# Kernel optimization log

Measured on AMD Instinct MI355X. Metric: run time of the kernel, lower is better.

## Reference

```python
import jax, jax.numpy as jnp
import numpy as np
import math

B, S, HID, H = 2, 4096, 512, 8
D_K = HID // H


def setup_inputs() -> dict:
    key = jax.random.key(0)
    ks = jax.random.split(key, 8)
    inp = {
        "query": jax.random.normal(ks[0], (B, S, HID), dtype=jnp.float32),
        "key": jax.random.normal(ks[1], (B, S, HID), dtype=jnp.float32),
        "value": jax.random.normal(ks[2], (B, S, HID), dtype=jnp.float32),
        "mask": jax.random.randint(ks[3], (B, S), 0, 2, dtype=jnp.int32),
        # conv1d kernel_size=1, bias=False -> plain [out,in] weights (xavier-normal-ish)
        "Wq": jax.random.normal(ks[4], (HID, HID), dtype=jnp.float32) * (1.0 / math.sqrt(HID)),
        "Wk": jax.random.normal(ks[5], (HID, HID), dtype=jnp.float32) * (1.0 / math.sqrt(HID)),
        "Wv": jax.random.normal(ks[6], (HID, HID), dtype=jnp.float32) * (1.0 / math.sqrt(HID)),
        "Wo": jax.random.normal(ks[7], (HID, HID), dtype=jnp.float32) * (1.0 / math.sqrt(HID)),
    }
    return inp


def reference(query, key, value, mask, Wq, Wk, Wv, Wo):
    b, s, _ = query.shape
    # conv1d(k=1, bias=False) projection == x @ W.T; split heads -> [b,h,s,d_k]
    def proj(x, W):
        return jnp.einsum('bsd,ed->bse', x, W).reshape(b, s, H, D_K).transpose(0, 2, 1, 3)
    q, k, v = proj(query, Wq), proj(key, Wk), proj(value, Wv)
    # NOTE: original scales by 1/log(d_k), not 1/sqrt(d_k)
    score = jnp.einsum('bhqd,bhkd->bhqk', q, k) / math.log(D_K)
    m = mask.reshape(b, 1, 1, s)  # broadcast over heads and query positions
    score = jnp.where(m == 0, jnp.float32(-1e30), score)
    attn = jax.nn.softmax(score, axis=-1)  # dropout is identity in eval
    x = jnp.einsum('bhqk,bhkd->bhqd', attn, v)
    x = x.transpose(0, 2, 1, 3).reshape(b, s, HID)
    return jnp.einsum('bsd,ed->bse', x, Wo)
```

## Files before the change

kernel.cpp:

```cpp
#include <hip/hip_runtime.h>
#include <hip/hip_bf16.h>
#include <cstdint>
#include <cstddef>


namespace {

constexpr int kB = 2, kS = 4096, kHid = 512, kH = 8, kDk = 64;
constexpr int kBH = kB * kH;
constexpr int kM = kB * kS;

typedef __attribute__((ext_vector_type(8))) short short8;
typedef __attribute__((ext_vector_type(4))) float floatx4;
typedef __attribute__((ext_vector_type(16))) float floatx16;
typedef __attribute__((ext_vector_type(4))) unsigned int uintx4;
typedef unsigned short u16;

__device__ __forceinline__ u16 bf16rne(float f) {
    uint32_t u = __float_as_uint(f);
    u += 0x7fffu + ((u >> 16) & 1u);
    return (u16)(u >> 16);
}
__device__ __forceinline__ uint32_t pk2(float lo, float hi) {
#if __has_builtin(__builtin_amdgcn_cvt_pk_bf16_f32)
    typedef __attribute__((ext_vector_type(2))) __bf16 bf2;
    bf2 h = __builtin_amdgcn_cvt_pk_bf16_f32(lo, hi);
    return __builtin_bit_cast(uint32_t, h);
#else
    return ((uint32_t)bf16rne(hi) << 16) | (uint32_t)bf16rne(lo);
#endif
}
__device__ __forceinline__ float fexp2(float x) {
#if __has_builtin(__builtin_amdgcn_exp2f)
    return __builtin_amdgcn_exp2f(x);
#else
    return exp2f(x);
#endif
}
__device__ __forceinline__ float bf2f(u16 v) {
    return __uint_as_float((uint32_t)v << 16);
}
__device__ __forceinline__ void plswap(uint32_t& a, uint32_t& b) {
#if __has_builtin(__builtin_amdgcn_permlane32_swap)
    typedef __attribute__((ext_vector_type(2))) unsigned int uint2v;
    uint2v r = __builtin_amdgcn_permlane32_swap(a, b, false, false);
    a = r[0]; b = r[1];
#else
    asm volatile("v_permlane32_swap_b32 %0, %1" : "+v"(a), "+v"(b));
#endif
}
__device__ __forceinline__ void gload16(const void* g, void* l) {
    __builtin_amdgcn_global_load_lds(
        (const __attribute__((address_space(1))) void*)g,
        (__attribute__((address_space(3))) void*)l, 16, 0, 0);
}

__global__ __launch_bounds__(256) void cvt_qw(const float* __restrict__ q,
    const float* __restrict__ k, const float* __restrict__ v,
    const float* __restrict__ w0, const float* __restrict__ w1,
    const float* __restrict__ w2, const float* __restrict__ w3,
    u16* __restrict__ xall, u16* __restrict__ wall) {
    const int bx = blockIdx.x;
    if (bx < 12288) {
        int z = bx >> 12;
        size_t i = (size_t)(bx & 4095) * 256 + threadIdx.x;
        const float* src = z == 0 ? q : (z == 1 ? k : v);
        float4 f = ((const float4*)src)[i];
        ushort4 o;
        o.x = bf16rne(f.x); o.y = bf16rne(f.y);
        o.z = bf16rne(f.z); o.w = bf16rne(f.w);
        ((ushort4*)(xall + (size_t)z * kM * kHid))[i] = o;
    } else {
        int r = bx - 12288;
        int z = r >> 8;
        size_t i = (size_t)(r & 255) * 256 + threadIdx.x;
        const float* src = z == 0 ? w0 : (z == 1 ? w1 : (z == 2 ? w2 : w3));
        float sc = (z == 0)
            ? (float)(1.4426950408889634 / (6.0 * 0.6931471805599453))
            : 1.0f;
        float4 f = ((const float4*)src)[i];
        ushort4 o;
        o.x = bf16rne(f.x * sc); o.y = bf16rne(f.y * sc);
        o.z = bf16rne(f.z * sc); o.w = bf16rne(f.w * sc);
        ((ushort4*)(wall + (size_t)z * kHid * kHid))[i] = o;
    }
}

__global__ __launch_bounds__(256) void cvt_mask(const int* __restrict__ mask,
    float* __restrict__ fb) {
    int i = blockIdx.x * 256 + threadIdx.x;
    fb[i] = mask[i] ? 0.0f : -1e30f;
}

__global__ __launch_bounds__(256, 3) void proj(const u16* __restrict__ xall,
    const u16* __restrict__ wall, u16* __restrict__ qp, u16* __restrict__ kp,
    u16* __restrict__ vt) {
    __shared__ float smt[4][16][68];
    const int z = blockIdx.z;
    const u16* x = xall + (size_t)z * kM * kHid;
    const u16* w = wall + (size_t)z * kHid * kHid;
    const int wv = threadIdx.x >> 6, lane = threadIdx.x & 63;
    const int quad = lane >> 4, l16 = lane & 15;
    const int mb = blockIdx.y * 128 + (wv >> 1) * 64;
    const int nb = blockIdx.x * 128 + (wv & 1) * 64;
    floatx4 acc[4][4] = {};
    const u16* xr = x + (size_t)(mb + l16) * kHid + quad * 8;
    const u16* wr = w + (size_t)(nb + l16) * kHid + quad * 8;
    for (int k0 = 0; k0 < kHid; k0 += 32) {
        short8 a[4], bt[4];
#pragma unroll
        for (int i = 0; i < 4; i++)
            a[i] = *(const short8*)(xr + (size_t)i * 16 * kHid + k0);
#pragma unroll
        for (int t = 0; t < 4; t++)
            bt[t] = *(const short8*)(wr + (size_t)t * 16 * kHid + k0);
#pragma unroll
        for (int i = 0; i < 4; i++)
#pragma unroll
        for (int t = 0; t < 4; t++)
            acc[i][t] = __builtin_amdgcn_mfma_f32_16x16x32_bf16(a[i], bt[t], acc[i][t], 0, 0, 0);
    }
    if (z < 2) {
        u16* dst = (z == 0) ? qp : kp;
        const int row16 = lane >> 2, cseg = (lane & 3) * 16;
#pragma unroll
        for (int i = 0; i < 4; i++) {
#pragma unroll
            for (int t = 0; t < 4; t++)
#pragma unroll
            for (int r = 0; r < 4; r++)
                smt[wv][quad * 4 + r][t * 16 + l16] = acc[i][t][r];
            __builtin_amdgcn_wave_barrier();
            const float* rp = &smt[wv][row16][cseg];
            float4 f0 = *(const float4*)(rp);
            float4 f1 = *(const float4*)(rp + 4);
            float4 f2 = *(const float4*)(rp + 8);
            float4 f3 = *(const float4*)(rp + 12);
            uint4 o0, o1;
            o0.x = pk2(f0.x, f0.y); o0.y = pk2(f0.z, f0.w);
            o0.z = pk2(f1.x, f1.y); o0.w = pk2(f1.z, f1.w);
            o1.x = pk2(f2.x, f2.y); o1.y = pk2(f2.z, f2.w);
            o1.z = pk2(f3.x, f3.y); o1.w = pk2(f3.z, f3.w);
            u16* dp = dst + (size_t)(mb + i * 16 + row16) * kHid + nb + cseg;
            *(uint4*)dp = o0;
            *(uint4*)(dp + 8) = o1;
            __builtin_amdgcn_wave_barrier();
        }
    } else {
#pragma unroll
        for (int i = 0; i < 4; i++)
#pragma unroll
        for (int t = 0; t < 4; t++) {
            int m0 = mb + i * 16 + quad * 4;
            int n = nb + t * 16 + l16;
            int b = m0 >> 12, s = m0 & (kS - 1);
            int h = n >> 6,   d = n & (kDk - 1);
            ushort4 o;
            o.x = bf16rne(acc[i][t][0]); o.y = bf16rne(acc[i][t][1]);
            o.z = bf16rne(acc[i][t][2]); o.w = bf16rne(acc[i][t][3]);
            *(ushort4*)(vt + ((size_t)(b * kH + h) * kDk + d) * kS + s) = o;
        }
    }
}

__global__ __launch_bounds__(256, 4) void attn(const u16* __restrict__ qp,
    const u16* __restrict__ kp, const u16* __restrict__ vt,
    const float* __restrict__ fbias, u16* __restrict__ ows,
    float* __restrict__ rsws) {
    union SmT {
        struct { u16 K[2][64][64]; u16 V[2][64][64]; } s;
        float ep[4][32][33];
    };
    __shared__ __align__(16) SmT sm;
    const int tid = threadIdx.x;
    const int wv = tid >> 6, l = tid & 63;
    const int hf = l >> 5, q32 = l & 31, l7 = l & 7;
    const int bh = blockIdx.y, b = bh >> 3, h = bh & 7;
    const int kz = blockIdx.z;
    const int q0 = blockIdx.x * 128 + wv * 32;
    const u16* Qb = qp + (size_t)b * kS * kHid + h * 64;
    const u16* Kb = kp + (size_t)b * kS * kHid + h * 64;
    const u16* Vb = vt + (size_t)bh * kDk * kS;
    const float* fm = fbias + b * kS;

    short8 qf[4];
#pragma unroll
    for (int m = 0; m < 4; m++)
        qf[m] = *(const short8*)(Qb + (size_t)(q0 + q32) * kHid + m * 16 + hf * 8);

    floatx16 O0 = {}, O1 = {};
    float rs = 0.0f;

    const int srow = l >> 3;
    const int swcol = (l7 ^ srow) * 8;
    auto stage = [&](int itn, int ph) {
        const size_t kr = (size_t)(itn * 64 + wv * 8 + srow);
        gload16(Kb + kr * kHid + swcol,        &sm.s.K[ph][wv * 8][0]);
        gload16(Kb + (kr + 32) * kHid + swcol, &sm.s.K[ph][wv * 8 + 32][0]);
        const size_t vr = (size_t)(wv * 8 + srow) * kS + itn * 64 + swcol;
        gload16(Vb + vr,                       &sm.s.V[ph][wv * 8][0]);
        gload16(Vb + (size_t)32 * kS + vr,     &sm.s.V[ph][wv * 8 + 32][0]);
    };

    stage(kz, 0);
    __syncthreads();

    for (int s = 0; s < 32; ++s) {
        const int it = kz + 2 * s, ph = s & 1, kt = it * 64;
        if (s < 31) stage(it + 2, ph ^ 1);
#pragma unroll
        for (int ks = 0; ks < 2; ++ks) {
            short8 kf[4];
#pragma unroll
            for (int m = 0; m < 4; m++)
                kf[m] = *(const short8*)&sm.s.K[ph][ks * 32 + q32][((2 * m + hf) ^ l7) * 8];
            short8 vf[2][2];
#pragma unroll
            for (int ds = 0; ds < 2; ds++)
#pragma unroll
            for (int tt = 0; tt < 2; tt++)
                vf[ds][tt] = *(const short8*)&sm.s.V[ph][ds * 32 + q32][((ks * 4 + tt * 2 + hf) ^ l7) * 8];
            floatx16 st;
            {
                const float* fp = fm + kt + ks * 32 + 4 * hf;
                float4 g0 = *(const float4*)(fp);
                float4 g1 = *(const float4*)(fp + 8);
                float4 g2 = *(const float4*)(fp + 16);
                float4 g3 = *(const float4*)(fp + 24);
                st[0] = g0.x;  st[1] = g0.y;  st[2] = g0.z;  st[3] = g0.w;
                st[4] = g1.x;  st[5] = g1.y;  st[6] = g1.z;  st[7] = g1.w;
                st[8] = g2.x;  st[9] = g2.y;  st[10] = g2.z; st[11] = g2.w;
                st[12] = g3.x; st[13] = g3.y; st[14] = g3.z; st[15] = g3.w;
            }
#pragma unroll
            for (int m = 0; m < 4; m++)
                st = __builtin_amdgcn_mfma_f32_32x32x16_bf16(kf[m], qf[m], st, 0, 0, 0);
            float xx[16];
#pragma unroll
            for (int r = 0; r < 16; r++) xx[r] = fexp2(st[r]);
            rs += (((xx[0] + xx[1]) + (xx[2] + xx[3])) + ((xx[4] + xx[5]) + (xx[6] + xx[7])))
                + (((xx[8] + xx[9]) + (xx[10] + xx[11])) + ((xx[12] + xx[13]) + (xx[14] + xx[15])));
            uint32_t w00 = pk2(xx[0], xx[1]),   w01 = pk2(xx[2], xx[3]);
            uint32_t w10 = pk2(xx[4], xx[5]),   w11 = pk2(xx[6], xx[7]);
            uint32_t w20 = pk2(xx[8], xx[9]),   w21 = pk2(xx[10], xx[11]);
            uint32_t w30 = pk2(xx[12], xx[13]), w31 = pk2(xx[14], xx[15]);
            plswap(w00, w10); plswap(w01, w11);
            plswap(w20, w30); plswap(w21, w31);
            uintx4 t0 = {w00, w01, w10, w11};
            uintx4 t1 = {w20, w21, w30, w31};
            short8 bf0 = __builtin_bit_cast(short8, t0);
            short8 bf1 = __builtin_bit_cast(short8, t1);
            O0 = __builtin_amdgcn_mfma_f32_32x32x16_bf16(vf[0][0], bf0, O0, 0, 0, 0);
            O0 = __builtin_amdgcn_mfma_f32_32x32x16_bf16(vf[0][1], bf1, O0, 0, 0, 0);
            O1 = __builtin_amdgcn_mfma_f32_32x32x16_bf16(vf[1][0], bf0, O1, 0, 0, 0);
            O1 = __builtin_amdgcn_mfma_f32_32x32x16_bf16(vf[1][1], bf1, O1, 0, 0, 0);
        }
        __syncthreads();
    }

    rs += __shfl_xor(rs, 32);
    if (hf == 0)
        rsws[((size_t)kz * kBH + bh) * kS + q0 + q32] = rs;

    u16* Ob = ows + (((size_t)kz * kBH + bh) * kS + q0) * kDk;
#pragma unroll
    for (int ds = 0; ds < 2; ds++) {
#pragma unroll
        for (int r = 0; r < 16; r++)
            sm.ep[wv][q32][(r & 3) + 8 * (r >> 2) + 4 * hf] = (ds == 0) ? O0[r] : O1[r];
        __builtin_amdgcn_wave_barrier();
        {
            const int qq = l >> 1, c0 = (l & 1) * 16;
            float f[16];
#pragma unroll
            for (int j = 0; j < 16; j++) f[j] = sm.ep[wv][qq][c0 + j];
            uint4 o0, o1;
            o0.x = pk2(f[0], f[1]);   o0.y = pk2(f[2], f[3]);
            o0.z = pk2(f[4], f[5]);   o0.w = pk2(f[6], f[7]);
            o1.x = pk2(f[8], f[9]);   o1.y = pk2(f[10], f[11]);
            o1.z = pk2(f[12], f[13]); o1.w = pk2(f[14], f[15]);
            u16* dp = Ob + (size_t)qq * kDk + ds * 32 + c0;
            *(uint4*)dp = o0;
            *(uint4*)(dp + 8) = o1;
        }
        __builtin_amdgcn_wave_barrier();
    }
}

__global__ __launch_bounds__(256) void combine(const u16* __restrict__ ows,
    const float* __restrict__ rsws, u16* __restrict__ xo) {
    size_t i = (size_t)blockIdx.x * 256 + threadIdx.x;
    const int d8 = (int)(i & 7);
    const int s  = (int)((i >> 3) & (kS - 1));
    const int bh = (int)(i >> 15);
    const int b = bh >> 3, h = bh & 7;
    const size_t base = ((size_t)bh * kS + s) * kDk + d8 * 8;
    short8 a = *(const short8*)(ows + base);
    short8 c = *(const short8*)(ows + (size_t)kBH * kS * kDk + base);
    float r = rsws[(size_t)bh * kS + s] + rsws[(size_t)kBH * kS + (size_t)bh * kS + s];
    float inv = 1.0f / r;
    float e[8];
#pragma unroll
    for (int j = 0; j < 8; j++)
        e[j] = (bf2f((u16)a[j]) + bf2f((u16)c[j])) * inv;
    uint4 o;
    o.x = pk2(e[0], e[1]); o.y = pk2(e[2], e[3]);
    o.z = pk2(e[4], e[5]); o.w = pk2(e[6], e[7]);
    *(uint4*)(xo + ((size_t)b * kS + s) * kHid + h * 64 + d8 * 8) = o;
}

__global__ __launch_bounds__(256, 3) void oproj(const u16* __restrict__ x,
    const u16* __restrict__ w, float* __restrict__ out) {
    const int wv = threadIdx.x >> 6, lane = threadIdx.x & 63;
    const int quad = lane >> 4, l16 = lane & 15;
    const int mb = blockIdx.y * 128 + (wv >> 1) * 64;
    const int nb = blockIdx.x * 128 + (wv & 1) * 64;
    floatx4 acc[4][4] = {};
    const u16* xr = x + (size_t)(mb + l16) * kHid + quad * 8;
    const u16* wr = w + (size_t)(nb + l16) * kHid + quad * 8;
    for (int k0 = 0; k0 < kHid; k0 += 32) {
        short8 a[4], bt[4];
#pragma unroll
        for (int i = 0; i < 4; i++)
            a[i] = *(const short8*)(xr + (size_t)i * 16 * kHid + k0);
#pragma unroll
        for (int t = 0; t < 4; t++)
            bt[t] = *(const short8*)(wr + (size_t)t * 16 * kHid + k0);
#pragma unroll
        for (int i = 0; i < 4; i++)
#pragma unroll
        for (int t = 0; t < 4; t++)
            acc[i][t] = __builtin_amdgcn_mfma_f32_16x16x32_bf16(a[i], bt[t], acc[i][t], 0, 0, 0);
    }
#pragma unroll
    for (int i = 0; i < 4; i++)
#pragma unroll
    for (int t = 0; t < 4; t++)
#pragma unroll
    for (int r = 0; r < 4; r++) {
        int m = mb + i * 16 + quad * 4 + r;
        int n = nb + t * 16 + l16;
        out[(size_t)m * kHid + n] = acc[i][t][r];
    }
}

}

extern "C" void kernel_launch(void* const* d_in, const int* in_sizes, int n_in,
                              void* d_out, int out_size, void* d_ws, size_t ws_size,
                              hipStream_t stream) {
    const float* q  = (const float*)d_in[0];
    const float* k  = (const float*)d_in[1];
    const float* v  = (const float*)d_in[2];
    const int* mask = (const int*)d_in[3];
    const float* w0 = (const float*)d_in[4];
    const float* w1 = (const float*)d_in[5];
    const float* w2 = (const float*)d_in[6];
    const float* w3 = (const float*)d_in[7];
    float* out = (float*)d_out;

    u16* ws   = (u16*)d_ws;
    u16* xall = ws;
    u16* wall = xall + (size_t)3 * kM * kHid;
    u16* qp   = wall + (size_t)4 * kHid * kHid;
    u16* kp   = qp + (size_t)kBH * kS * kDk;
    u16* vt   = kp + (size_t)kBH * kS * kDk;
    u16* ows  = xall;
    float* fbias = (float*)(xall + (size_t)2 * kM * kHid);
    float* rsws  = fbias + (size_t)kB * kS;
    u16* xo   = qp;

    dim3 blk(256);
    cvt_qw <<<dim3(13312), blk, 0, stream>>>(q, k, v, w0, w1, w2, w3, xall, wall);
    proj   <<<dim3(kHid / 128, kM / 128, 3), blk, 0, stream>>>(xall, wall, qp, kp, vt);
    cvt_mask<<<dim3(kB * kS / 256), blk, 0, stream>>>(mask, fbias);
    attn   <<<dim3(kS / 128, kBH, 2), blk, 0, stream>>>(qp, kp, vt, fbias, ows, rsws);
    combine<<<dim3(2048), blk, 0, stream>>>(ows, rsws, xo);
    oproj  <<<dim3(kHid / 128, kM / 128), blk, 0, stream>>>(
        xo, wall + (size_t)3 * kHid * kHid, out);
}
```

Measured before the change: 268.4 us.

## Process two query tiles per wave in attention to reuse K/V fragments

Each wave now handles 64 query rows (two 32-row tiles) instead of 32, so every K/V tile staged in shared memory and every fragment read from LDS serves twice as many MFMA ops. The grid is flattened to 512 blocks with a remapped block index that interleaves heads and places the two key-split halves in separate block ranges. Stage pointers are advanced incrementally rather than recomputed. In exchange, register pressure roughly doubles, occupancy drops to 2 blocks per CU, and the grid is halved.

```diff
diff --git a/kernel.cpp b/kernel.cpp
--- a/kernel.cpp
+++ b/kernel.cpp
@@ -163,7 +163,7 @@
     }
 }
 
-__global__ __launch_bounds__(256, 4) void attn(const u16* __restrict__ qp,
+__global__ __launch_bounds__(256, 2) void attn(const u16* __restrict__ qp,
     const u16* __restrict__ kp, const u16* __restrict__ vt,
     const float* __restrict__ fbias, u16* __restrict__ ows,
     float* __restrict__ rsws) {
@@ -175,39 +175,47 @@
     const int tid = threadIdx.x;
     const int wv = tid >> 6, l = tid & 63;
     const int hf = l >> 5, q32 = l & 31, l7 = l & 7;
-    const int bh = blockIdx.y, b = bh >> 3, h = bh & 7;
-    const int kz = blockIdx.z;
-    const int q0 = blockIdx.x * 128 + wv * 32;
+    const int wg = blockIdx.x;
+    const int bh = ((wg & 7) << 1) | ((wg >> 3) & 1);
+    const int qb = (wg >> 4) & 15;
+    const int kz = wg >> 8;
+    const int b = bh >> 3, h = bh & 7;
+    const int qbase = qb * 256 + wv * 64;
     const u16* Qb = qp + (size_t)b * kS * kHid + h * 64;
     const u16* Kb = kp + (size_t)b * kS * kHid + h * 64;
     const u16* Vb = vt + (size_t)bh * kDk * kS;
     const float* fm = fbias + b * kS;
 
-    short8 qf[4];
+    short8 qf[2][4];
+#pragma unroll
+    for (int qt = 0; qt < 2; qt++)
 #pragma unroll
     for (int m = 0; m < 4; m++)
-        qf[m] = *(const short8*)(Qb + (size_t)(q0 + q32) * kHid + m * 16 + hf * 8);
-
-    floatx16 O0 = {}, O1 = {};
-    float rs = 0.0f;
+        qf[qt][m] = *(const short8*)(Qb + (size_t)(qbase + qt * 32 + q32) * kHid + m * 16 + hf * 8);
+
+    floatx16 O[2][2] = {};
+    float rs[2] = {0.0f, 0.0f};
 
     const int srow = l >> 3;
-    const int swcol = (l7 ^ srow) * 8;
-    auto stage = [&](int itn, int ph) {
-        const size_t kr = (size_t)(itn * 64 + wv * 8 + srow);
-        gload16(Kb + kr * kHid + swcol,        &sm.s.K[ph][wv * 8][0]);
-        gload16(Kb + (kr + 32) * kHid + swcol, &sm.s.K[ph][wv * 8 + 32][0]);
-        const size_t vr = (size_t)(wv * 8 + srow) * kS + itn * 64 + swcol;
-        gload16(Vb + vr,                       &sm.s.V[ph][wv * 8][0]);
-        gload16(Vb + (size_t)32 * kS + vr,     &sm.s.V[ph][wv * 8 + 32][0]);
+    const int pcol = (l7 ^ srow) * 8;
+    const u16* pK = Kb + (size_t)(kz * 64 + wv * 8 + srow) * kHid + pcol;
+    const u16* pV = Vb + (size_t)(wv * 8 + srow) * kS + kz * 64 + pcol;
+    auto stage = [&](int ph) {
+        gload16(pK,                        &sm.s.K[ph][wv * 8][0]);
+        gload16(pK + (size_t)32 * kHid,    &sm.s.K[ph][wv * 8 + 32][0]);
+        gload16(pV,                        &sm.s.V[ph][wv * 8][0]);
+        gload16(pV + (size_t)32 * kS,      &sm.s.V[ph][wv * 8 + 32][0]);
+        pK += (size_t)128 * kHid;
+        pV += 128;
     };
 
-    stage(kz, 0);
+    stage(0);
     __syncthreads();
 
-    for (int s = 0; s < 32; ++s) {
-        const int it = kz + 2 * s, ph = s & 1, kt = it * 64;
-        if (s < 31) stage(it + 2, ph ^ 1);
+    for (int s5 = 0; s5 < 32; ++s5) {
+        const int ph = s5 & 1;
+        const int kt = (kz + 2 * s5) * 64;
+        if (s5 < 31) stage(ph ^ 1);
 #pragma unroll
         for (int ks = 0; ks < 2; ++ks) {
             short8 kf[4];
@@ -220,70 +228,74 @@
 #pragma unroll
             for (int tt = 0; tt < 2; tt++)
                 vf[ds][tt] = *(const short8*)&sm.s.V[ph][ds * 32 + q32][((ks * 4 + tt * 2 + hf) ^ l7) * 8];
-            floatx16 st;
-            {
-                const float* fp = fm + kt + ks * 32 + 4 * hf;
-                float4 g0 = *(const float4*)(fp);
-                float4 g1 = *(const float4*)(fp + 8);
-                float4 g2 = *(const float4*)(fp + 16);
-                float4 g3 = *(const float4*)(fp + 24);
+            const float* fp = fm + kt + ks * 32 + 4 * hf;
+            float4 g0 = *(const float4*)(fp);
+            float4 g1 = *(const float4*)(fp + 8);
+            float4 g2 = *(const float4*)(fp + 16);
+            float4 g3 = *(const float4*)(fp + 24);
+#pragma unroll
+            for (int qt = 0; qt < 2; ++qt) {
+                floatx16 st;
                 st[0] = g0.x;  st[1] = g0.y;  st[2] = g0.z;  st[3] = g0.w;
                 st[4] = g1.x;  st[5] = g1.y;  st[6] = g1.z;  st[7] = g1.w;
                 st[8] = g2.x;  st[9] = g2.y;  st[10] = g2.z; st[11] = g2.w;
                 st[12] = g3.x; st[13] = g3.y; st[14] = g3.z; st[15] = g3.w;
+#pragma unroll
+                for (int m = 0; m < 4; m++)
+                    st = __builtin_amdgcn_mfma_f32_32x32x16_bf16(kf[m], qf[qt][m], st, 0, 0, 0);
+                float xx[16];
+#pragma unroll
+                for (int r = 0; r < 16; r++) xx[r] = fexp2(st[r]);
+                rs[qt] += (((xx[0] + xx[1]) + (xx[2] + xx[3])) + ((xx[4] + xx[5]) + (xx[6] + xx[7])))
+                        + (((xx[8] + xx[9]) + (xx[10] + xx[11])) + ((xx[12] + xx[13]) + (xx[14] + xx[15])));
+                uint32_t w00 = pk2(xx[0], xx[1]),   w01 = pk2(xx[2], xx[3]);
+                uint32_t w10 = pk2(xx[4], xx[5]),   w11 = pk2(xx[6], xx[7]);
+                uint32_t w20 = pk2(xx[8], xx[9]),   w21 = pk2(xx[10], xx[11]);
+                uint32_t w30 = pk2(xx[12], xx[13]), w31 = pk2(xx[14], xx[15]);
+                plswap(w00, w10); plswap(w01, w11);
+                plswap(w20, w30); plswap(w21, w31);
+                uintx4 t0 = {w00, w01, w10, w11};
+                uintx4 t1 = {w20, w21, w30, w31};
+                short8 bf0 = __builtin_bit_cast(short8, t0);
+                short8 bf1 = __builtin_bit_cast(short8, t1);
+                O[qt][0] = __builtin_amdgcn_mfma_f32_32x32x16_bf16(vf[0][0], bf0, O[qt][0], 0, 0, 0);
+                O[qt][0] = __builtin_amdgcn_mfma_f32_32x32x16_bf16(vf[0][1], bf1, O[qt][0], 0, 0, 0);
+                O[qt][1] = __builtin_amdgcn_mfma_f32_32x32x16_bf16(vf[1][0], bf0, O[qt][1], 0, 0, 0);
+                O[qt][1] = __builtin_amdgcn_mfma_f32_32x32x16_bf16(vf[1][1], bf1, O[qt][1], 0, 0, 0);
             }
-#pragma unroll
-            for (int m = 0; m < 4; m++)
-                st = __builtin_amdgcn_mfma_f32_32x32x16_bf16(kf[m], qf[m], st, 0, 0, 0);
-            float xx[16];
-#pragma unroll
-            for (int r = 0; r < 16; r++) xx[r] = fexp2(st[r]);
-            rs += (((xx[0] + xx[1]) + (xx[2] + xx[3])) + ((xx[4] + xx[5]) + (xx[6] + xx[7])))
-                + (((xx[8] + xx[9]) + (xx[10] + xx[11])) + ((xx[12] + xx[13]) + (xx[14] + xx[15])));
-            uint32_t w00 = pk2(xx[0], xx[1]),   w01 = pk2(xx[2], xx[3]);
-            uint32_t w10 = pk2(xx[4], xx[5]),   w11 = pk2(xx[6], xx[7]);
-            uint32_t w20 = pk2(xx[8], xx[9]),   w21 = pk2(xx[10], xx[11]);
-            uint32_t w30 = pk2(xx[12], xx[13]), w31 = pk2(xx[14], xx[15]);
-            plswap(w00, w10); plswap(w01, w11);
-            plswap(w20, w30); plswap(w21, w31);
-            uintx4 t0 = {w00, w01, w10, w11};
-            uintx4 t1 = {w20, w21, w30, w31};
-            short8 bf0 = __builtin_bit_cast(short8, t0);
-            short8 bf1 = __builtin_bit_cast(short8, t1);
-            O0 = __builtin_amdgcn_mfma_f32_32x32x16_bf16(vf[0][0], bf0, O0, 0, 0, 0);
-            O0 = __builtin_amdgcn_mfma_f32_32x32x16_bf16(vf[0][1], bf1, O0, 0, 0, 0);
-            O1 = __builtin_amdgcn_mfma_f32_32x32x16_bf16(vf[1][0], bf0, O1, 0, 0, 0);
-            O1 = __builtin_amdgcn_mfma_f32_32x32x16_bf16(vf[1][1], bf1, O1, 0, 0, 0);
         }
         __syncthreads();
     }
 
-    rs += __shfl_xor(rs, 32);
-    if (hf == 0)
-        rsws[((size_t)kz * kBH + bh) * kS + q0 + q32] = rs;
-
-    u16* Ob = ows + (((size_t)kz * kBH + bh) * kS + q0) * kDk;
-#pragma unroll
-    for (int ds = 0; ds < 2; ds++) {
-#pragma unroll
-        for (int r = 0; r < 16; r++)
-            sm.ep[wv][q32][(r & 3) + 8 * (r >> 2) + 4 * hf] = (ds == 0) ? O0[r] : O1[r];
-        __builtin_amdgcn_wave_barrier();
-        {
-            const int qq = l >> 1, c0 = (l & 1) * 16;
-            float f[16];
-#pragma unroll
-            for (int j = 0; j < 16; j++) f[j] = sm.ep[wv][qq][c0 + j];
-            uint4 o0, o1;
-            o0.x = pk2(f[0], f[1]);   o0.y = pk2(f[2], f[3]);
-            o0.z = pk2(f[4], f[5]);   o0.w = pk2(f[6], f[7]);
-            o1.x = pk2(f[8], f[9]);   o1.y = pk2(f[10], f[11]);
-            o1.z = pk2(f[12], f[13]); o1.w = pk2(f[14], f[15]);
-            u16* dp = Ob + (size_t)qq * kDk + ds * 32 + c0;
-            *(uint4*)dp = o0;
-            *(uint4*)(dp + 8) = o1;
+#pragma unroll
+    for (int qt = 0; qt < 2; ++qt) {
+        float r = rs[qt];
+        r += __shfl_xor(r, 32);
+        if (hf == 0)
+            rsws[((size_t)kz * kBH + bh) * kS + qbase + qt * 32 + q32] = r;
+        u16* Ob = ows + (((size_t)kz * kBH + bh) * kS + qbase + qt * 32) * kDk;
+#pragma unroll
+        for (int ds = 0; ds < 2; ds++) {
+#pragma unroll
+            for (int rr = 0; rr < 16; rr++)
+                sm.ep[wv][q32][(rr & 3) + 8 * (rr >> 2) + 4 * hf] = O[qt][ds][rr];
+            __builtin_amdgcn_wave_barrier();
+            {
+                const int qq = l >> 1, c0 = (l & 1) * 16;
+                float f[16];
+#pragma unroll
+                for (int j = 0; j < 16; j++) f[j] = sm.ep[wv][qq][c0 + j];
+                uint4 o0, o1;
+                o0.x = pk2(f[0], f[1]);   o0.y = pk2(f[2], f[3]);
+                o0.z = pk2(f[4], f[5]);   o0.w = pk2(f[6], f[7]);
+                o1.x = pk2(f[8], f[9]);   o1.y = pk2(f[10], f[11]);
+                o1.z = pk2(f[12], f[13]); o1.w = pk2(f[14], f[15]);
+                u16* dp = Ob + (size_t)qq * kDk + ds * 32 + c0;
+                *(uint4*)dp = o0;
+                *(uint4*)(dp + 8) = o1;
+            }
+            __builtin_amdgcn_wave_barrier();
         }
-        __builtin_amdgcn_wave_barrier();
     }
 }
 
@@ -374,7 +386,7 @@
     cvt_qw <<<dim3(13312), blk, 0, stream>>>(q, k, v, w0, w1, w2, w3, xall, wall);
     proj   <<<dim3(kHid / 128, kM / 128, 3), blk, 0, stream>>>(xall, wall, qp, kp, vt);
     cvt_mask<<<dim3(kB * kS / 256), blk, 0, stream>>>(mask, fbias);
-    attn   <<<dim3(kS / 128, kBH, 2), blk, 0, stream>>>(qp, kp, vt, fbias, ows, rsws);
+    attn   <<<dim3(512), blk, 0, stream>>>(qp, kp, vt, fbias, ows, rsws);
     combine<<<dim3(2048), blk, 0, stream>>>(ows, rsws, xo);
     oproj  <<<dim3(kHid / 128, kM / 128), blk, 0, stream>>>(
         xo, wall + (size_t)3 * kHid * kHid, out);
```

Result: no change. 264.9 us (-1.3%).
